# Kernel tuning notes

Measured on AMD Instinct MI355X. Metric: run time of the kernel, lower is better.

## Reference

```python
import jax, jax.numpy as jnp
import numpy as np

NUM_EXPERTS = 8
IN_FEATURES = 1024
OUT_FEATURES = 1024
TOP_K = 2


def setup_inputs() -> dict:
    key = jax.random.key(0)
    k_x, k_we, k_be, k_wg, k_bg = jax.random.split(key, 5)
    scale_e = 1.0 / np.sqrt(IN_FEATURES)
    x = jax.random.normal(k_x, (4, 2048, IN_FEATURES), dtype=jnp.float32)
    # expert weights stored torch-style [E, out, in], bias [E, out]
    W_experts = jax.random.uniform(k_we, (NUM_EXPERTS, OUT_FEATURES, IN_FEATURES), minval=-scale_e, maxval=scale_e, dtype=jnp.float32)
    b_experts = jax.random.uniform(k_be, (NUM_EXPERTS, OUT_FEATURES), minval=-scale_e, maxval=scale_e, dtype=jnp.float32)
    W_gate = jax.random.uniform(k_wg, (NUM_EXPERTS, IN_FEATURES), minval=-scale_e, maxval=scale_e, dtype=jnp.float32)
    b_gate = jax.random.uniform(k_bg, (NUM_EXPERTS,), minval=-scale_e, maxval=scale_e, dtype=jnp.float32)
    return {"x": x, "W_experts": W_experts, "b_experts": b_experts, "W_gate": W_gate, "b_gate": b_gate}


def reference(x, W_experts, b_experts, W_gate, b_gate):
    B, S, D = x.shape
    x_flat = x.reshape(-1, D)  # [T, D]
    # gating
    gate_logits = x_flat @ W_gate.T + b_gate  # [T, E]
    topk_vals, topk_idxs = jax.lax.top_k(gate_logits, TOP_K)  # [T, K]
    topk_weights = jax.nn.softmax(topk_vals, axis=-1)  # [T, K]
    # dense per-token per-expert weight via one-hot scatter of top-k weights
    one_hot = jax.nn.one_hot(topk_idxs, NUM_EXPERTS, dtype=x.dtype)  # [T, K, E]
    w = jnp.einsum('tke,tk->te', one_hot, topk_weights)  # [T, E]
    # every expert runs densely over all tokens (faithful to source)
    expert_outs = jnp.einsum('td,efd->tef', x_flat, W_experts) + b_experts  # [T, E, F]
    out_flat = jnp.einsum('te,tef->tf', w, expert_outs)  # [T, F]
    return out_flat.reshape(B, S, -1)
```

## Files before the change

kernel.cpp:

```cpp
#include <hip/hip_runtime.h>
#include <hip/hip_bf16.h>
#include <stdint.h>

#define NE 8
#define DK 1024
#define FN 1024
#define NTOK 8192

#define BN 256
#define BK 64
#define NIT (DK / BK)
#define H 144

#define HB 32
#define EPB (NTOK * 2 / HB)

#define BUFS 73728
#define BOFF 40960

#define GATE_BLOCKS (NTOK / 4)
#define CONV_BLOCKS (NE * FN * DK / 4 / 256)

typedef __attribute__((ext_vector_type(4))) float f32x4;
typedef __attribute__((ext_vector_type(8))) short short8;
typedef __attribute__((ext_vector_type(4))) short short4v;

__device__ __forceinline__ unsigned short f2bf(float f) {
    union { float f; unsigned u; } v; v.f = f;
    unsigned r = v.u;
    unsigned lsb = (r >> 16) & 1u;
    r += 0x7fffu + lsb;
    return (unsigned short)(r >> 16);
}
__device__ __forceinline__ float bf2f(unsigned short u) {
    union { unsigned u; float f; } v; v.u = ((unsigned)u) << 16;
    return v.f;
}

__global__ __launch_bounds__(256) void k_prep(const float* __restrict__ x,
    const float* __restrict__ Wg, const float* __restrict__ bg,
    const float* __restrict__ W,
    unsigned short* __restrict__ xb, unsigned short* __restrict__ Wb,
    int* __restrict__ meta_e, float* __restrict__ meta_w)
{
    if (blockIdx.x >= GATE_BLOCKS) {
        int i = (blockIdx.x - GATE_BLOCKS) * 256 + threadIdx.x;
        f32x4 v = ((const f32x4*)W)[i];
        short4v b;
        b.x = (short)f2bf(v.x); b.y = (short)f2bf(v.y);
        b.z = (short)f2bf(v.z); b.w = (short)f2bf(v.w);
        ((short4v*)Wb)[i] = b;
        return;
    }

    const int lane = threadIdx.x & 63;
    const int t = blockIdx.x * 4 + (threadIdx.x >> 6);

    const f32x4* xr = (const f32x4*)(x + (size_t)t * DK);
    f32x4 xv[4];
#pragma unroll
    for (int c = 0; c < 4; ++c) xv[c] = xr[lane + 64 * c];

    short4v* xbo = (short4v*)(xb + (size_t)t * DK);
#pragma unroll
    for (int c = 0; c < 4; ++c) {
        short4v b;
        b.x = (short)f2bf(xv[c].x); b.y = (short)f2bf(xv[c].y);
        b.z = (short)f2bf(xv[c].z); b.w = (short)f2bf(xv[c].w);
        xbo[lane + 64 * c] = b;
    }

    float acc[NE];
#pragma unroll
    for (int e = 0; e < NE; ++e) {
        const f32x4* wr = (const f32x4*)(Wg + e * DK);
        float a = 0.f;
#pragma unroll
        for (int c = 0; c < 4; ++c) {
            f32x4 wv = wr[lane + 64 * c];
            a += xv[c].x * wv.x + xv[c].y * wv.y + xv[c].z * wv.z + xv[c].w * wv.w;
        }
        acc[e] = a;
    }
#pragma unroll
    for (int e = 0; e < NE; ++e) {
        float a = acc[e];
#pragma unroll
        for (int off = 32; off > 0; off >>= 1) a += __shfl_xor(a, off, 64);
        acc[e] = a;
    }
    if (lane == 0) {
        float v[NE];
#pragma unroll
        for (int e = 0; e < NE; ++e) v[e] = acc[e] + bg[e];
        int b0 = 0; float m0 = v[0];
#pragma unroll
        for (int e = 1; e < NE; ++e) if (v[e] > m0) { m0 = v[e]; b0 = e; }
        int b1 = -1; float m1 = -3.4e38f;
#pragma unroll
        for (int e = 0; e < NE; ++e) if (e != b0 && v[e] > m1) { m1 = v[e]; b1 = e; }
        float r = expf(m1 - m0);
        float s = 1.f + r;
        meta_e[2 * t] = b0; meta_e[2 * t + 1] = b1;
        meta_w[2 * t] = 1.f / s; meta_w[2 * t + 1] = r / s;
    }
}

__global__ __launch_bounds__(256) void k_hist(const int* __restrict__ meta_e,
                                              int* __restrict__ blockcnt)
{
    __shared__ int lh[NE];
    if (threadIdx.x < NE) lh[threadIdx.x] = 0;
    __syncthreads();
    int base = blockIdx.x * EPB;
#pragma unroll
    for (int k = 0; k < EPB / 256; ++k)
        atomicAdd(&lh[meta_e[base + k * 256 + threadIdx.x]], 1);
    __syncthreads();
    if (threadIdx.x < NE) blockcnt[blockIdx.x * NE + threadIdx.x] = lh[threadIdx.x];
}

__global__ __launch_bounds__(256) void k_scatter(const int* __restrict__ meta_e,
    const float* __restrict__ meta_w, const int* __restrict__ blockcnt,
    int* __restrict__ seg, int* __restrict__ ridx, float* __restrict__ rw)
{
    __shared__ int lh[NE];
    __shared__ int bb[NE];
    __shared__ int colsum[NE];
    __shared__ int segstart[NE];
    int tid = threadIdx.x;
    if (tid < NE) {
        lh[tid] = 0;
        int run = 0, mypre = 0;
        for (int b = 0; b < HB; ++b) {
            if (b == (int)blockIdx.x) mypre = run;
            run += blockcnt[b * NE + tid];
        }
        colsum[tid] = run;
        bb[tid] = mypre;
    }
    __syncthreads();
    if (tid == 0) {
        int s = 0;
        for (int e = 0; e < NE; ++e) { segstart[e] = s; s += colsum[e]; }
        if (blockIdx.x == 0) {
            int s2 = 0;
            for (int e = 0; e < NE; ++e) { seg[e] = s2; s2 += colsum[e]; }
            seg[NE] = s2;
        }
    }
    __syncthreads();
    if (tid < NE) bb[tid] += segstart[tid];
    __syncthreads();
    int bs = blockIdx.x * EPB;
#pragma unroll
    for (int k = 0; k < EPB / 256; ++k) {
        int i = bs + k * 256 + tid;
        int e = meta_e[i];
        int r = atomicAdd(&lh[e], 1);
        int p = bb[e] + r;
        ridx[p] = i;
        rw[p] = meta_w[i];
    }
}

template <int MODE>
__global__ __launch_bounds__(512, 2) void k_gemm(const unsigned short* __restrict__ xb,
    const unsigned short* __restrict__ Wb, const float* __restrict__ be,
    const int* __restrict__ seg, const int* __restrict__ ridx,
    const float* __restrict__ rw, float* __restrict__ out, void* __restrict__ ywv)
{
    __shared__ char Lds[2 * BUFS];

    const int bid = blockIdx.x;
    const int e = bid & 7;
    const int n0 = ((bid >> 3) & 3) * BN;
    const int mt = bid >> 5;
    const int s0 = seg[e];
    const int L = seg[e + 1] - s0;
    const int lpt = (L + 7) >> 3;
    int m0 = mt * lpt;
    const int m_end = (m0 + lpt < L) ? (m0 + lpt) : L;
    if (m0 >= m_end) return;

    const int tid = threadIdx.x;
    const int lane = tid & 63;
    const int wid = tid >> 6;
    const int wm = wid >> 2, wn = wid & 3;
    const int frow = lane & 15;
    const int fq = lane >> 4;

    const int bgr = ((tid & 3) ^ ((tid >> 3) & 3)) * 8;
    unsigned boff[2];
#pragma unroll
    for (int c = 0; c < 2; ++c)
        boff[c] = (((unsigned)(e * FN + n0 + c * 128 + (tid >> 2))) << 10) + bgr;

    int b_base[2];
    {
        int r = wn * 64 + frow;
        int sl = fq ^ ((frow >> 1) & 3);
#pragma unroll
        for (int kk = 0; kk < 2; ++kk)
            b_base[kk] = BOFF + kk * 16384 + r * 64 + sl * 16;
    }
    int a_base[2];
#pragma unroll
    for (int kk = 0; kk < 2; ++kk)
        a_base[kk] = (wm * H + frow) * 128 + (((kk * 4 + fq) ^ (frow & 7)) * 16);

    char* LB = (char*)Lds;
    const int ag = ((tid & 7) ^ ((tid >> 3) & 7)) * 8;

    for (; m0 < m_end; m0 += 288) {
        unsigned aoff[5];
#pragma unroll
        for (int c = 0; c < 5; ++c) {
            int r = c * 64 + (tid >> 3);
            int idx = m0 + r; if (idx >= m_end) idx = m_end - 1;
            aoff[c] = (((unsigned)(ridx[s0 + idx] >> 1)) << 10) + ag;
        }

        f32x4 acc[9][4];
#pragma unroll
        for (int i = 0; i < 9; ++i)
#pragma unroll
            for (int j = 0; j < 4; ++j) acc[i][j] = f32x4{0.f, 0.f, 0.f, 0.f};

        auto STAGE_A = [&](int buf, int kt) {
            const unsigned ko = kt * BK;
            char* dst = LB + buf * BUFS + wid * 1024;
#pragma unroll
            for (int c = 0; c < 5; ++c)
                __builtin_amdgcn_global_load_lds(
                    (const __attribute__((address_space(1))) void*)(xb + aoff[c] + ko),
                    (__attribute__((address_space(3))) void*)(dst + c * 8192), 16, 0, 0);
        };
        auto STAGE_B = [&](int buf, int kt, int kh) {
            const unsigned ko = kt * BK + kh * 32;
            char* dst = LB + buf * BUFS + BOFF + kh * 16384 + wid * 1024;
#pragma unroll
            for (int c = 0; c < 2; ++c)
                __builtin_amdgcn_global_load_lds(
                    (const __attribute__((address_space(1))) void*)(Wb + boff[c] + ko),
                    (__attribute__((address_space(3))) void*)(dst + c * 8192), 16, 0, 0);
        };

#define GATE(N) do { asm volatile("s_waitcnt vmcnt(" #N ")" ::: "memory"); \
                     __builtin_amdgcn_s_barrier(); \
                     __builtin_amdgcn_sched_barrier(0); } while (0)
#define BARP  do { __builtin_amdgcn_s_barrier(); \
                   __builtin_amdgcn_sched_barrier(0); } while (0)
#define LGKM0 do { asm volatile("s_waitcnt lgkmcnt(0)" ::: "memory"); \
                   __builtin_amdgcn_sched_barrier(0); } while (0)
#define MFMA45(AF, BF, MLO, CNT) do { \
    __builtin_amdgcn_s_setprio(1); \
    _Pragma("unroll") \
    for (int mi = 0; mi < (CNT); ++mi) { \
        _Pragma("unroll") \
        for (int ni = 0; ni < 4; ++ni) \
            acc[(MLO) + mi][ni] = __builtin_amdgcn_mfma_f32_16x16x32_bf16( \
                AF[mi], BF[ni], acc[(MLO) + mi][ni], 0, 0, 0); \
    } \
    __builtin_amdgcn_s_setprio(0); } while (0)

        STAGE_A(0, 0); STAGE_B(0, 0, 0); STAGE_B(0, 0, 1);
        __builtin_amdgcn_sched_barrier(0);

        for (int t = 0; t < NIT; ++t) {
            const int b = t & 1;
            const char* Cb = LB + b * BUFS;
            const bool st = (t + 1 < NIT);
            short8 bf[4], af[5];

            GATE(2);
#pragma unroll
            for (int ni = 0; ni < 4; ++ni)
                bf[ni] = *(const short8*)(Cb + b_base[0] + ni * 1024);
#pragma unroll
            for (int mi = 0; mi < 5; ++mi)
                af[mi] = *(const short8*)(Cb + a_base[0] + mi * 2048);
            if (st) STAGE_A(b ^ 1, t + 1);
            LGKM0;
            MFMA45(af, bf, 0, 5);

            BARP;
#pragma unroll
            for (int mi = 0; mi < 4; ++mi)
                af[mi] = *(const short8*)(Cb + a_base[0] + (5 + mi) * 2048);
            if (st) STAGE_B(b ^ 1, t + 1, 0);
            LGKM0;
            MFMA45(af, bf, 5, 4);

            if (st) { GATE(7); } else { GATE(0); }
#pragma unroll
            for (int ni = 0; ni < 4; ++ni)
                bf[ni] = *(const short8*)(Cb + b_base[1] + ni * 1024);
#pragma unroll
            for (int mi = 0; mi < 5; ++mi)
                af[mi] = *(const short8*)(Cb + a_base[1] + mi * 2048);
            if (st) STAGE_B(b ^ 1, t + 1, 1);
            LGKM0;
            MFMA45(af, bf, 0, 5);

            BARP;
#pragma unroll
            for (int mi = 0; mi < 4; ++mi)
                af[mi] = *(const short8*)(Cb + a_base[1] + (5 + mi) * 2048);
            LGKM0;
            MFMA45(af, bf, 5, 4);
        }
#undef GATE
#undef BARP
#undef LGKM0
#undef MFMA45

        float bias_n[4];
#pragma unroll
        for (int ni = 0; ni < 4; ++ni)
            bias_n[ni] = be[e * FN + n0 + wn * 64 + ni * 16 + frow];

        const int fq4 = fq * 4;
#pragma unroll
        for (int mi = 0; mi < 9; ++mi) {
#pragma unroll
            for (int j = 0; j < 4; ++j) {
                int lr = mi * 16 + fq4 + j;
                int idx = m0 + wm * H + lr;
                if (idx < m_end) {
                    float w = rw[s0 + idx];
                    int oi = ridx[s0 + idx];
                    if (MODE == 0) {
                        float* orow = out + (size_t)(oi >> 1) * FN + n0 + wn * 64 + frow;
#pragma unroll
                        for (int ni = 0; ni < 4; ++ni)
                            atomicAdd(orow + ni * 16, w * (acc[mi][ni][j] + bias_n[ni]));
                    } else if (MODE == 1) {
                        short4v pk;
                        pk.x = (short)f2bf(w * (acc[mi][0][j] + bias_n[0]));
                        pk.y = (short)f2bf(w * (acc[mi][1][j] + bias_n[1]));
                        pk.z = (short)f2bf(w * (acc[mi][2][j] + bias_n[2]));
                        pk.w = (short)f2bf(w * (acc[mi][3][j] + bias_n[3]));
                        *(short4v*)((unsigned short*)ywv + (size_t)oi * FN + n0 + wn * 64 + frow * 4) = pk;
                    } else {
                        f32x4 pk;
                        pk.x = w * (acc[mi][0][j] + bias_n[0]);
                        pk.y = w * (acc[mi][1][j] + bias_n[1]);
                        pk.z = w * (acc[mi][2][j] + bias_n[2]);
                        pk.w = w * (acc[mi][3][j] + bias_n[3]);
                        *(f32x4*)((float*)ywv + (size_t)oi * FN + n0 + wn * 64 + frow * 4) = pk;
                    }
                }
            }
        }
    }
}

__global__ __launch_bounds__(256) void k_combine_bf(const unsigned short* __restrict__ yw,
                                                    float* __restrict__ out)
{
    __shared__ float ls[FN];
    int t = blockIdx.x, i = threadIdx.x;
    const unsigned* r0 = (const unsigned*)(yw + (size_t)(2 * t) * FN);
    const unsigned* r1 = (const unsigned*)(yw + (size_t)(2 * t + 1) * FN);
    unsigned a0 = r0[2 * i], a1 = r0[2 * i + 1];
    unsigned c0 = r1[2 * i], c1 = r1[2 * i + 1];
    float s0 = bf2f((unsigned short)(a0 & 0xffff)) + bf2f((unsigned short)(c0 & 0xffff));
    float s1 = bf2f((unsigned short)(a0 >> 16))    + bf2f((unsigned short)(c0 >> 16));
    float s2 = bf2f((unsigned short)(a1 & 0xffff)) + bf2f((unsigned short)(c1 & 0xffff));
    float s3 = bf2f((unsigned short)(a1 >> 16))    + bf2f((unsigned short)(c1 >> 16));
    int base = (i >> 4) * 64 + (i & 15);
    ls[base +  0] = s0;
    ls[base + 16] = s1;
    ls[base + 32] = s2;
    ls[base + 48] = s3;
    __syncthreads();
    ((f32x4*)(out + (size_t)t * FN))[i] = ((const f32x4*)ls)[i];
}

__global__ __launch_bounds__(256) void k_combine_f32(const float* __restrict__ yw,
                                                     float* __restrict__ out)
{
    __shared__ float ls[FN];
    int t = blockIdx.x, i = threadIdx.x;
    f32x4 a = ((const f32x4*)(yw + (size_t)(2 * t) * FN))[i];
    f32x4 b = ((const f32x4*)(yw + (size_t)(2 * t + 1) * FN))[i];
    f32x4 s = a + b;
    int base = (i >> 4) * 64 + (i & 15);
    ls[base +  0] = s.x;
    ls[base + 16] = s.y;
    ls[base + 32] = s.z;
    ls[base + 48] = s.w;
    __syncthreads();
    ((f32x4*)(out + (size_t)t * FN))[i] = ((const f32x4*)ls)[i];
}

extern "C" void kernel_launch(void* const* d_in, const int* in_sizes, int n_in,
                              void* d_out, int out_size, void* d_ws, size_t ws_size,
                              hipStream_t stream)
{
    const float* x   = (const float*)d_in[0];
    const float* We  = (const float*)d_in[1];
    const float* beb = (const float*)d_in[2];
    const float* Wg  = (const float*)d_in[3];
    const float* bg  = (const float*)d_in[4];
    float* out = (float*)d_out;

    char* ws = (char*)d_ws;
    unsigned short* xb = (unsigned short*)ws;
    unsigned short* Wb = (unsigned short*)(ws + (size_t)(16 << 20));
    size_t off = (size_t)(32 << 20);
    int*   seg      = (int*)(ws + off);   off += 256;
    int*   blockcnt = (int*)(ws + off);   off += HB * NE * 4;
    int*   meta_e   = (int*)(ws + off);   off += (size_t)NTOK * 2 * 4;
    float* meta_w   = (float*)(ws + off); off += (size_t)NTOK * 2 * 4;
    int*   ridxb    = (int*)(ws + off);   off += (size_t)NTOK * 2 * 4;
    float* rwb      = (float*)(ws + off); off += (size_t)NTOK * 2 * 4;
    void*  yw       = (void*)(ws + ((off + 255) & ~(size_t)255));
    size_t yw_base  = (size_t)((off + 255) & ~(size_t)255);

    int mode;
    if (ws_size >= yw_base + (size_t)NTOK * 2 * FN * 2) mode = 1;
    else if (ws_size >= yw_base + (size_t)NTOK * 2 * FN * 4) mode = 2;
    else mode = 0;

    k_prep<<<GATE_BLOCKS + CONV_BLOCKS, 256, 0, stream>>>(x, Wg, bg, We, xb, Wb,
                                                          meta_e, meta_w);
    k_hist<<<HB, 256, 0, stream>>>(meta_e, blockcnt);
    k_scatter<<<HB, 256, 0, stream>>>(meta_e, meta_w, blockcnt, seg, ridxb, rwb);

    const int nblk = NE * (FN / BN) * 8;
    if (mode == 1) {
        k_gemm<1><<<nblk, 512, 0, stream>>>(xb, Wb, beb, seg, ridxb, rwb, out, yw);
        k_combine_bf<<<NTOK, 256, 0, stream>>>((const unsigned short*)yw, out);
    } else if (mode == 2) {
        k_gemm<2><<<nblk, 512, 0, stream>>>(xb, Wb, beb, seg, ridxb, rwb, out, yw);
        k_combine_f32<<<NTOK, 256, 0, stream>>>((const float*)yw, out);
    } else {
        hipMemsetAsync(d_out, 0, (size_t)NTOK * FN * 4, stream);
        k_gemm<0><<<nblk, 512, 0, stream>>>(xb, Wb, beb, seg, ridxb, rwb, out, yw);
    }
}
```

Measured before the change: 80.54 us.

## Issue next-tile prefetch before LDS reads, widen combine and weight-convert blocks

The GEMM main loop now issues the global-to-LDS prefetch for the next K tile right after each barrier, before the fragment reads from LDS. It also drops the sched_barrier after the barriers so the compiler can interleave instructions more freely. The weight fp32-to-bf16 conversion now handles two vectors per thread, halving the number of conversion blocks. The combine kernels process two tokens per 512-thread block instead of one token per 256-thread block. The aim is better overlap of memory traffic with MFMA work and less launch and scheduling overhead, at the risk of altered instruction ordering around the waits.

After: 80.87 us. Within noise of the previous version (+0.4%).

```diff
diff --git a/kernel.cpp b/kernel.cpp
--- a/kernel.cpp
+++ b/kernel.cpp
@@ -19,7 +19,7 @@
 #define BOFF 40960
 
 #define GATE_BLOCKS (NTOK / 4)
-#define CONV_BLOCKS (NE * FN * DK / 4 / 256)
+#define CONV_BLOCKS (NE * FN * DK / 8 / 256)
 
 typedef __attribute__((ext_vector_type(4))) float f32x4;
 typedef __attribute__((ext_vector_type(8))) short short8;
@@ -44,12 +44,15 @@
     int* __restrict__ meta_e, float* __restrict__ meta_w)
 {
     if (blockIdx.x >= GATE_BLOCKS) {
-        int i = (blockIdx.x - GATE_BLOCKS) * 256 + threadIdx.x;
-        f32x4 v = ((const f32x4*)W)[i];
-        short4v b;
-        b.x = (short)f2bf(v.x); b.y = (short)f2bf(v.y);
-        b.z = (short)f2bf(v.z); b.w = (short)f2bf(v.w);
-        ((short4v*)Wb)[i] = b;
+        int i = ((blockIdx.x - GATE_BLOCKS) * 256 + threadIdx.x) * 2;
+#pragma unroll
+        for (int q = 0; q < 2; ++q) {
+            f32x4 v = ((const f32x4*)W)[i + q];
+            short4v b;
+            b.x = (short)f2bf(v.x); b.y = (short)f2bf(v.y);
+            b.z = (short)f2bf(v.z); b.w = (short)f2bf(v.w);
+            ((short4v*)Wb)[i + q] = b;
+        }
         return;
     }
 
@@ -247,10 +250,8 @@
         };
 
 #define GATE(N) do { asm volatile("s_waitcnt vmcnt(" #N ")" ::: "memory"); \
-                     __builtin_amdgcn_s_barrier(); \
-                     __builtin_amdgcn_sched_barrier(0); } while (0)
-#define BARP  do { __builtin_amdgcn_s_barrier(); \
-                   __builtin_amdgcn_sched_barrier(0); } while (0)
+                     __builtin_amdgcn_s_barrier(); } while (0)
+#define BARP  __builtin_amdgcn_s_barrier()
 #define LGKM0 do { asm volatile("s_waitcnt lgkmcnt(0)" ::: "memory"); \
                    __builtin_amdgcn_sched_barrier(0); } while (0)
 #define MFMA45(AF, BF, MLO, CNT) do { \
@@ -274,32 +275,32 @@
             short8 bf[4], af[5];
 
             GATE(2);
+            if (st) STAGE_A(b ^ 1, t + 1);
 #pragma unroll
             for (int ni = 0; ni < 4; ++ni)
                 bf[ni] = *(const short8*)(Cb + b_base[0] + ni * 1024);
 #pragma unroll
             for (int mi = 0; mi < 5; ++mi)
                 af[mi] = *(const short8*)(Cb + a_base[0] + mi * 2048);
-            if (st) STAGE_A(b ^ 1, t + 1);
             LGKM0;
             MFMA45(af, bf, 0, 5);
 
             BARP;
+            if (st) STAGE_B(b ^ 1, t + 1, 0);
 #pragma unroll
             for (int mi = 0; mi < 4; ++mi)
                 af[mi] = *(const short8*)(Cb + a_base[0] + (5 + mi) * 2048);
-            if (st) STAGE_B(b ^ 1, t + 1, 0);
             LGKM0;
             MFMA45(af, bf, 5, 4);
 
             if (st) { GATE(7); } else { GATE(0); }
+            if (st) STAGE_B(b ^ 1, t + 1, 1);
 #pragma unroll
             for (int ni = 0; ni < 4; ++ni)
                 bf[ni] = *(const short8*)(Cb + b_base[1] + ni * 1024);
 #pragma unroll
             for (int mi = 0; mi < 5; ++mi)
                 af[mi] = *(const short8*)(Cb + a_base[1] + mi * 2048);
-            if (st) STAGE_B(b ^ 1, t + 1, 1);
             LGKM0;
             MFMA45(af, bf, 0, 5);
 
@@ -356,11 +357,13 @@
     }
 }
 
-__global__ __launch_bounds__(256) void k_combine_bf(const unsigned short* __restrict__ yw,
+__global__ __launch_bounds__(512) void k_combine_bf(const unsigned short* __restrict__ yw,
                                                     float* __restrict__ out)
 {
-    __shared__ float ls[FN];
-    int t = blockIdx.x, i = threadIdx.x;
+    __shared__ float ls[2][FN];
+    int t = blockIdx.x * 2 + (threadIdx.x >> 8);
+    int i = threadIdx.x & 255;
+    int half = threadIdx.x >> 8;
     const unsigned* r0 = (const unsigned*)(yw + (size_t)(2 * t) * FN);
     const unsigned* r1 = (const unsigned*)(yw + (size_t)(2 * t + 1) * FN);
     unsigned a0 = r0[2 * i], a1 = r0[2 * i + 1];
@@ -370,29 +373,31 @@
     float s2 = bf2f((unsigned short)(a1 & 0xffff)) + bf2f((unsigned short)(c1 & 0xffff));
     float s3 = bf2f((unsigned short)(a1 >> 16))    + bf2f((unsigned short)(c1 >> 16));
     int base = (i >> 4) * 64 + (i & 15);
-    ls[base +  0] = s0;
-    ls[base + 16] = s1;
-    ls[base + 32] = s2;
-    ls[base + 48] = s3;
-    __syncthreads();
-    ((f32x4*)(out + (size_t)t * FN))[i] = ((const f32x4*)ls)[i];
-}
-
-__global__ __launch_bounds__(256) void k_combine_f32(const float* __restrict__ yw,
+    ls[half][base +  0] = s0;
+    ls[half][base + 16] = s1;
+    ls[half][base + 32] = s2;
+    ls[half][base + 48] = s3;
+    __syncthreads();
+    ((f32x4*)(out + (size_t)t * FN))[i] = ((const f32x4*)&ls[half][0])[i];
+}
+
+__global__ __launch_bounds__(512) void k_combine_f32(const float* __restrict__ yw,
                                                      float* __restrict__ out)
 {
-    __shared__ float ls[FN];
-    int t = blockIdx.x, i = threadIdx.x;
+    __shared__ float ls[2][FN];
+    int t = blockIdx.x * 2 + (threadIdx.x >> 8);
+    int i = threadIdx.x & 255;
+    int half = threadIdx.x >> 8;
     f32x4 a = ((const f32x4*)(yw + (size_t)(2 * t) * FN))[i];
     f32x4 b = ((const f32x4*)(yw + (size_t)(2 * t + 1) * FN))[i];
     f32x4 s = a + b;
     int base = (i >> 4) * 64 + (i & 15);
-    ls[base +  0] = s.x;
-    ls[base + 16] = s.y;
-    ls[base + 32] = s.z;
-    ls[base + 48] = s.w;
-    __syncthreads();
-    ((f32x4*)(out + (size_t)t * FN))[i] = ((const f32x4*)ls)[i];
+    ls[half][base +  0] = s.x;
+    ls[half][base + 16] = s.y;
+    ls[half][base + 32] = s.z;
+    ls[half][base + 48] = s.w;
+    __syncthreads();
+    ((f32x4*)(out + (size_t)t * FN))[i] = ((const f32x4*)&ls[half][0])[i];
 }
 
 extern "C" void kernel_launch(void* const* d_in, const int* in_sizes, int n_in,
@@ -432,10 +437,10 @@
     const int nblk = NE * (FN / BN) * 8;
     if (mode == 1) {
         k_gemm<1><<<nblk, 512, 0, stream>>>(xb, Wb, beb, seg, ridxb, rwb, out, yw);
-        k_combine_bf<<<NTOK, 256, 0, stream>>>((const unsigned short*)yw, out);
+        k_combine_bf<<<NTOK / 2, 512, 0, stream>>>((const unsigned short*)yw, out);
     } else if (mode == 2) {
         k_gemm<2><<<nblk, 512, 0, stream>>>(xb, Wb, beb, seg, ridxb, rwb, out, yw);
-        k_combine_f32<<<NTOK, 256, 0, stream>>>((const float*)yw, out);
+        k_combine_f32<<<NTOK / 2, 512, 0, stream>>>((const float*)yw, out);
     } else {
         hipMemsetAsync(d_out, 0, (size_t)NTOK * FN * 4, stream);
         k_gemm<0><<<nblk, 512, 0, stream>>>(xb, Wb, beb, seg, ridxb, rwb, out, yw);
```
